# Performance work log

Measured on AMD Instinct MI355X. Metric: run time of the kernel, lower is better.

The kernel has to match this reference:

```python
import jax, jax.numpy as jnp
import numpy as np

B, N, D, HID, OUT = 4, 6144, 64, 512, 64
FINE_CONF = 0.25


def setup_inputs() -> dict:
    key = jax.random.key(0)
    ks = jax.random.split(key, 16)

    def unit(k, shape):
        v = jax.random.normal(k, shape, dtype=jnp.float32)
        return v / jnp.linalg.norm(v, axis=-1, keepdims=True)

    def lin(k, fan_in, shape):
        return jax.random.normal(k, shape, dtype=jnp.float32) * (1.0 / np.sqrt(fan_in))

    return {
        'feats1': unit(ks[0], (B, N, D)),
        'feats2': unit(ks[1], (B, N, D)),
        'kps1': jax.random.uniform(ks[2], (B, N, 2), dtype=jnp.float32) * 512.0,
        'kps2': jax.random.uniform(ks[3], (B, N, 2), dtype=jnp.float32) * 512.0,
        'scales1': jnp.ones((B, N), dtype=jnp.float32),
        'w1': lin(ks[4], 2 * D, (2 * D, HID)), 'b1': jnp.zeros((HID,), jnp.float32),
        'w2': lin(ks[5], HID, (HID, HID)),   'b2': jnp.zeros((HID,), jnp.float32),
        'w3': lin(ks[6], HID, (HID, HID)),   'b3': jnp.zeros((HID,), jnp.float32),
        'w4': lin(ks[7], HID, (HID, HID)),   'b4': jnp.zeros((HID,), jnp.float32),
        'w5': lin(ks[8], HID, (HID, OUT)),   'b5': jnp.zeros((OUT,), jnp.float32),
    }


def _fine_matcher(x, w1, b1, w2, b2, w3, b3, w4, b4, w5, b5):
    # eval-mode BN folded into the Linears -> plain MLP
    h = jax.nn.relu(x @ w1 + b1)
    h = jax.nn.relu(h @ w2 + b2)
    h = jax.nn.relu(h @ w3 + b3)
    h = jax.nn.relu(h @ w4 + b4)
    return h @ w5 + b5  # [B, N, 64]


def reference(feats1, feats2, kps1, kps2, scales1,
              w1, b1, w2, b2, w3, b3, w4, b4, w5, b5):
    # ---- batch_match: dense cosine sim + bidirectional argmax + mutual check ----
    cossim = jnp.einsum('bnd,bmd->bnm', feats1, feats2)       # [B, N, N]
    match12 = jnp.argmax(cossim, axis=-1)                      # [B, N]
    match21 = jnp.argmax(cossim, axis=1)                       # [B, N] (argmax over rows)
    idx0 = jnp.arange(match12.shape[1])
    back = jnp.take_along_axis(match21, match12, axis=1)       # match21[match12]
    mutual = back == idx0[None, :]                             # [B, N] bool

    # ---- refine_matches (masked instead of boolean compaction, jit-friendly) ----
    f2 = jnp.take_along_axis(feats2, match12[..., None], axis=1)   # [B, N, D]
    mkpts1 = jnp.take_along_axis(kps2, match12[..., None], axis=1) # [B, N, 2]
    offsets_raw = _fine_matcher(jnp.concatenate([feats1, f2], axis=-1),
                                w1, b1, w2, b2, w3, b3, w4, b4, w5, b5)  # [B, N, 64]

    # conf = softmax(3*offsets).max ; subpix uses softmax(3*offsets) too (temp=3)
    heat = jax.nn.softmax(3.0 * offsets_raw, axis=-1)          # [B, N, 64]
    conf = jnp.max(heat, axis=-1)                              # [B, N]

    hm = heat.reshape(heat.shape[0], heat.shape[1], 8, 8)      # [B, N, Hh, Wh]
    g = jnp.arange(8, dtype=heat.dtype) - 4.0                  # x - W//2 / y - H//2
    coords_x = jnp.sum(hm * g[None, None, None, :], axis=(-1, -2))
    coords_y = jnp.sum(hm * g[None, None, :, None], axis=(-1, -2))
    offsets = jnp.stack([coords_x, coords_y], axis=-1)         # [B, N, 2]

    mkpts0 = kps1 + offsets * scales1[..., None]
    matches = jnp.concatenate([mkpts0, mkpts1], axis=-1)       # [B, N, 4]
    mask_good = mutual & (conf > FINE_CONF)                    # valid-match mask
    return matches, mask_good
```

## Files before the change

### kernel.cpp

```cpp
#include <hip/hip_runtime.h>
#include <cstddef>
#include <cstdint>

#define BB 4
#define NN 6144
#define DD 64
#define HID 512
#define OUTD 64
#define CAP 512
#define RSPLIT 8

typedef unsigned long long ull;
typedef unsigned int u32;
typedef unsigned short u16;
typedef unsigned char u8;
typedef __attribute__((ext_vector_type(8))) short short8_t;
typedef __attribute__((ext_vector_type(4))) float floatx4;

#define OFF_ROWFIN 0
#define OFF_COLFIN 196608
#define OFF_WT     393216
#define OFF_F1T    2162688
#define OFF_F2T    5308416
#define OFF_RBM    8454144
#define OFF_CBM    10813440
#define OFF_CNTR   13172736
#define OFF_CNTC   13173504
#define OFF_LISTR  13174272
#define OFF_LISTC  13567488

#define WT1_OFF 0
#define WT2_OFF 65536
#define WT3_OFF 327680
#define WT4_OFF 589824
#define WT5_OFF 851968
#define WT_TOTAL 884736

__device__ __forceinline__ unsigned int fkey(float v) {
    unsigned int u = __float_as_uint(v);
    return (u & 0x80000000u) ? ~u : (u | 0x80000000u);
}

__device__ __forceinline__ float inv16(u32 k16) {
    u32 u = k16 << 16;
    return (u & 0x80000000u) ? __uint_as_float(u & 0x7fffffffu)
                             : __uint_as_float(~u);
}

__device__ __forceinline__ u16 f2bf(float f) {
    unsigned int u = __float_as_uint(f);
    u += 0x7FFFu + ((u >> 16) & 1u);
    return (u16)(u >> 16);
}

__device__ __forceinline__ u32 f2fp8x2(float a, float b) {
    return (u32)__builtin_amdgcn_cvt_pk_fp8_f32(a, b, 0, false) & 0xffffu;
}

__global__ __launch_bounds__(256) void prep_kernel(
    const float* __restrict__ w1, const float* __restrict__ w2,
    const float* __restrict__ w3, const float* __restrict__ w4,
    const float* __restrict__ w5,
    const float* __restrict__ f1, const float* __restrict__ f2,
    u8* __restrict__ wt8, u16* __restrict__ f1t, u16* __restrict__ f2t,
    ull* __restrict__ finals, int* __restrict__ cnts)
{
    int idx = blockIdx.x * 256 + threadIdx.x;

    if (idx < 2 * BB * NN) finals[idx] = 0ULL;
    if (idx < 384) cnts[idx] = 0;

    if (idx < WT_TOTAL) {
        const float* w; u8* o; int K, nsh, li;
        if (idx < 65536)        { w = w1; o = wt8 + WT1_OFF; K = 128; nsh = 9; li = idx; }
        else if (idx < 327680)  { w = w2; o = wt8 + WT2_OFF; K = 512; nsh = 9; li = idx - 65536; }
        else if (idx < 589824)  { w = w3; o = wt8 + WT3_OFF; K = 512; nsh = 9; li = idx - 327680; }
        else if (idx < 851968)  { w = w4; o = wt8 + WT4_OFF; K = 512; nsh = 9; li = idx - 589824; }
        else                    { w = w5; o = wt8 + WT5_OFF; K = 512; nsh = 6; li = idx - 851968; }
        int k = li >> nsh;
        int n = li & ((1 << nsh) - 1);
        u8 v = (u8)(f2fp8x2(w[li], 0.0f) & 0xff);
        int lane = (n & 15) | (((k >> 3) & 3) << 4);
        o[(((size_t)(n >> 4) * (K >> 5) + (k >> 5)) * 64 + lane) * 8 + (k & 7)] = v;
    }

    {
        const int TE = BB * NN * DD;
        const float* src; u16* dst; int e;
        if (idx < TE) { src = f1; dst = f1t; e = idx; }
        else          { src = f2; dst = f2t; e = idx - TE; }
        int k  = e & 63;
        int rn = e >> 6;
        int b  = rn / NN;
        int r  = rn - b * NN;
        int R  = r >> 7, rb = (r >> 4) & 7;
        int kb = k >> 5, lane = (r & 15) | (((k >> 3) & 3) << 4), j = k & 7;
        dst[(size_t)(b * 48 + R) * 8192 + ((rb * 2 + kb) * 64 + lane) * 8 + j] = f2bf(src[e]);
    }
}

__global__ __launch_bounds__(256, 2) void simb_kernel(
    const u16* __restrict__ f1t, const u16* __restrict__ f2t,
    u16* __restrict__ rbm, u16* __restrict__ cbm)
{
    __shared__ __align__(16) u16 sA[8192];
    __shared__ __align__(16) u16 sB[16384];
    __shared__ float cv[2][2][128];
    const int R = blockIdx.x, C2 = blockIdx.y, b = blockIdx.z;
    const int t = threadIdx.x, lane = t & 63, w = t >> 6;
    const int wr = w >> 1, wc = w & 1;
    const int l15 = lane & 15, l4 = lane >> 4;

    const u16* Ag = f1t + (size_t)(b * 48 + R) * 8192;
    const u16* Bg = f2t + (size_t)(b * 48 + C2 * 2) * 8192;

    #pragma unroll
    for (int rnd = 0; rnd < 4; ++rnd) {
        int c = rnd * 256 + t;
        *reinterpret_cast<uint4*>(&sA[c * 8]) = *reinterpret_cast<const uint4*>(Ag + c * 8);
    }
    #pragma unroll
    for (int rnd = 0; rnd < 8; ++rnd) {
        int c = rnd * 256 + t;
        *reinterpret_cast<uint4*>(&sB[c * 8]) = *reinterpret_cast<const uint4*>(Bg + c * 8);
    }
    __syncthreads();

    floatx4 acc[4][8];
    #pragma unroll
    for (int i = 0; i < 4; ++i)
        #pragma unroll
        for (int j = 0; j < 8; ++j) acc[i][j] = (floatx4)(0.0f);

    #pragma unroll
    for (int kb = 0; kb < 2; ++kb) {
        short8_t afr[4], bfr[8];
        #pragma unroll
        for (int i = 0; i < 4; ++i)
            afr[i] = *reinterpret_cast<const short8_t*>(
                &sA[(((wr * 4 + i) * 2 + kb) * 64 + lane) * 8]);
        #pragma unroll
        for (int j = 0; j < 8; ++j) {
            int cb = wc * 8 + j;
            bfr[j] = *reinterpret_cast<const short8_t*>(
                &sB[(cb >> 3) * 8192 + (((cb & 7) * 2 + kb) * 64 + lane) * 8]);
        }
        #pragma unroll
        for (int i = 0; i < 4; ++i)
            #pragma unroll
            for (int j = 0; j < 8; ++j)
                acc[i][j] = __builtin_amdgcn_mfma_f32_16x16x32_bf16(
                    afr[i], bfr[j], acc[i][j], 0, 0, 0);
    }

    const int Cme = C2 * 2 + wc;
    #pragma unroll
    for (int i = 0; i < 4; ++i) {
        #pragma unroll
        for (int reg = 0; reg < 4; ++reg) {
            float v = acc[i][0][reg];
            #pragma unroll
            for (int j = 1; j < 8; ++j) v = fmaxf(v, acc[i][j][reg]);
            v = fmaxf(v, __shfl_xor(v, 1));
            v = fmaxf(v, __shfl_xor(v, 2));
            v = fmaxf(v, __shfl_xor(v, 4));
            v = fmaxf(v, __shfl_xor(v, 8));
            if (l15 == 0) {
                int row = R * 128 + wr * 64 + i * 16 + l4 * 4 + reg;
                rbm[((size_t)b * NN + row) * 48 + Cme] = (u16)(fkey(v) >> 16);
            }
        }
    }

    #pragma unroll
    for (int j = 0; j < 8; ++j) {
        float v = acc[0][j][0];
        #pragma unroll
        for (int i = 0; i < 4; ++i)
            #pragma unroll
            for (int reg = 0; reg < 4; ++reg) v = fmaxf(v, acc[i][j][reg]);
        v = fmaxf(v, __shfl_xor(v, 16));
        v = fmaxf(v, __shfl_xor(v, 32));
        if (l4 == 0) cv[wc][wr][j * 16 + l15] = v;
    }
    __syncthreads();
    {
        int wcc = t >> 7, col0 = t & 127;
        float v = fmaxf(cv[wcc][0][col0], cv[wcc][1][col0]);
        int col = C2 * 256 + wcc * 128 + col0;
        cbm[((size_t)b * NN + col) * 48 + R] = (u16)(fkey(v) >> 16);
    }
}

__global__ __launch_bounds__(256) void scan_kernel(
    const u16* __restrict__ rbm, const u16* __restrict__ cbm,
    int* __restrict__ cntR, int* __restrict__ cntC,
    int* __restrict__ listR, int* __restrict__ listC)
{
    const u16* bm = blockIdx.y ? cbm : rbm;
    int* cnt  = blockIdx.y ? cntC : cntR;
    int* list = blockIdx.y ? listC : listR;

    __shared__ int lcnt[48];
    __shared__ int lbase[48];
    const int t = threadIdx.x;
    if (t < 48) lcnt[t] = 0;
    const int idx = blockIdx.x * 256 + t;
    const int b = (blockIdx.x * 256) / NN;
    const int n = idx - b * NN;

    u16 ks[48];
    const uint4* p4 = reinterpret_cast<const uint4*>(bm + (size_t)idx * 48);
    #pragma unroll
    for (int q = 0; q < 6; ++q) {
        uint4 u = p4[q];
        ks[q * 8 + 0] = (u16)(u.x & 0xffff); ks[q * 8 + 1] = (u16)(u.x >> 16);
        ks[q * 8 + 2] = (u16)(u.y & 0xffff); ks[q * 8 + 3] = (u16)(u.y >> 16);
        ks[q * 8 + 4] = (u16)(u.z & 0xffff); ks[q * 8 + 5] = (u16)(u.z >> 16);
        ks[q * 8 + 6] = (u16)(u.w & 0xffff); ks[q * 8 + 7] = (u16)(u.w >> 16);
    }
    u16 mx = 0;
    #pragma unroll
    for (int c = 0; c < 48; ++c) mx = ks[c] > mx ? ks[c] : mx;
    float thr = inv16(mx) - 0.010f;
    u32 m0 = 0, m1 = 0;
    #pragma unroll
    for (int c = 0; c < 48; ++c) {
        if (inv16((u32)ks[c] + 1) >= thr) {
            if (c < 32) m0 |= 1u << c; else m1 |= 1u << (c - 32);
        }
    }
    __syncthreads();
    {
        u32 a = m0;
        while (a) { int c = __builtin_ctz(a); a &= a - 1; atomicAdd(&lcnt[c], 1); }
        a = m1;
        while (a) { int c = 32 + __builtin_ctz(a); a &= a - 1; atomicAdd(&lcnt[c], 1); }
    }
    __syncthreads();
    if (t < 48) { lbase[t] = atomicAdd(&cnt[b * 48 + t], lcnt[t]); lcnt[t] = 0; }
    __syncthreads();
    {
        u32 a = m0;
        while (a) {
            int c = __builtin_ctz(a); a &= a - 1;
            int pos = lbase[c] + atomicAdd(&lcnt[c], 1);
            if (pos < CAP) list[(b * 48 + c) * CAP + pos] = n;
        }
        a = m1;
        while (a) {
            int c = 32 + __builtin_ctz(a); a &= a - 1;
            int pos = lbase[c] + atomicAdd(&lcnt[c], 1);
            if (pos < CAP) list[(b * 48 + c) * CAP + pos] = n;
        }
    }
}

__global__ __launch_bounds__(256, 2) void refine_kernel(
    const float* __restrict__ f1, const float* __restrict__ f2,
    const int* __restrict__ cntR, const int* __restrict__ cntC,
    const int* __restrict__ listR, const int* __restrict__ listC,
    ull* __restrict__ rowfin, ull* __restrict__ colfin)
{
    const float* qfeat = blockIdx.z ? f2 : f1;
    const float* tfeat = blockIdx.z ? f1 : f2;
    const int* cnt  = blockIdx.z ? cntC : cntR;
    const int* list = blockIdx.z ? listC : listR;
    ull* fin = blockIdx.z ? colfin : rowfin;

    const int b = blockIdx.x / 48;
    const int C = blockIdx.x - b * 48;
    const int sub = blockIdx.y;
    int n_items = cnt[b * 48 + C];
    if (n_items > CAP) n_items = CAP;
    int chunk = (n_items + RSPLIT - 1) / RSPLIT;
    int lo = sub * chunk;
    int hi = lo + chunk; if (hi > n_items) hi = n_items;
    if (lo >= hi) return;

    __shared__ float s2f[128 * 68];
    __shared__ float sq[16 * 68];
    const int t = threadIdx.x;
    const float* tb = tfeat + ((size_t)b * NN + C * 128) * 64;
    #pragma unroll
    for (int p = 0; p < 8; ++p) {
        int idx = p * 256 + t;
        int row = idx >> 4, c4 = idx & 15;
        *reinterpret_cast<float4*>(&s2f[row * 68 + c4 * 4]) =
            *reinterpret_cast<const float4*>(tb + row * 64 + c4 * 4);
    }
    __syncthreads();
    const int rs = t >> 4, cg = t & 15;
    const int* mylist = list + (b * 48 + C) * CAP;
    for (int base = lo; base < hi; base += 16) {
        {
            int lq = base + rs;
            int nn = (lq < hi) ? mylist[lq] : mylist[lo];
            *reinterpret_cast<float4*>(&sq[rs * 68 + cg * 4]) =
                *reinterpret_cast<const float4*>(qfeat + ((size_t)b * NN + nn) * 64 + cg * 4);
        }
        __syncthreads();

        int li = base + rs;
        bool valid = li < hi;
        int n = valid ? mylist[li] : mylist[lo];
        float dot[8];
        #pragma unroll
        for (int c8 = 0; c8 < 8; ++c8) dot[c8] = 0.0f;
        #pragma unroll 4
        for (int kq = 0; kq < 16; ++kq) {
            float4 a4 = *reinterpret_cast<const float4*>(&sq[rs * 68 + kq * 4]);
            #pragma unroll
            for (int c8 = 0; c8 < 8; ++c8) {
                float4 s4 = *reinterpret_cast<const float4*>(&s2f[(cg + 16 * c8) * 68 + kq * 4]);
                dot[c8] = fmaf(a4.x, s4.x, dot[c8]);
                dot[c8] = fmaf(a4.y, s4.y, dot[c8]);
                dot[c8] = fmaf(a4.z, s4.z, dot[c8]);
                dot[c8] = fmaf(a4.w, s4.w, dot[c8]);
            }
        }
        float bv = dot[0]; int bc = cg;
        #pragma unroll
        for (int c8 = 1; c8 < 8; ++c8) {
            if (dot[c8] > bv) { bv = dot[c8]; bc = cg + 16 * c8; }
        }
        ull pk = ((ull)fkey(bv) << 32) | (u32)(~(u32)(C * 128 + bc));
        ull qq;
        qq = __shfl_xor(pk, 1); pk = pk > qq ? pk : qq;
        qq = __shfl_xor(pk, 2); pk = pk > qq ? pk : qq;
        qq = __shfl_xor(pk, 4); pk = pk > qq ? pk : qq;
        qq = __shfl_xor(pk, 8); pk = pk > qq ? pk : qq;
        if (cg == 0 && valid) atomicMax(&fin[(size_t)b * NN + n], pk);
        __syncthreads();
    }
}


#define MLP_STEP(BUF, KB)                                                        \
    {                                                                            \
        const int kb2 = ((KB) + woff) & (NKB - 1);                               \
        __builtin_amdgcn_s_setprio(1);                                           \
        _Pragma("unroll")                                                        \
        for (int jb = 0; jb < 6; ++jb) {                                         \
            const int pt = jb * 16 + l15;                                        \
            const int sp = (kb2 * 4 + l4) ^ (pt & 7);                            \
            long bfr = *reinterpret_cast<const long*>(act + pt * 512 + sp * 8);  \
            _Pragma("unroll")                                                    \
            for (int ia = 0; ia < 4; ++ia)                                       \
                acc[ia][jb] = __builtin_amdgcn_mfma_f32_16x16x32_fp8_fp8(        \
                    BUF[ia], bfr, acc[ia][jb], 0, 0, 0);                         \
        }                                                                        \
        __builtin_amdgcn_s_setprio(0);                                           \
        if ((KB) + 3 < NKB) {                                                    \
            const int kbp = ((KB) + 3 + woff) & (NKB - 1);                       \
            _Pragma("unroll")                                                    \
            for (int ia = 0; ia < 4; ++ia)                                       \
                BUF[ia] = *reinterpret_cast<const long*>(                        \
                    wt8 + (((size_t)(chBlk0 + ia) * NKB + kbp) * 64 + lane) * 8);\
        }                                                                        \
    }

template<int K>
__device__ __forceinline__ void mlp_layer8(
    u8* act, const u8* __restrict__ wt8,
    const float* __restrict__ bias, int lane, int wid)
{
    constexpr int NKB = K / 32;
    floatx4 acc[4][6];
    #pragma unroll
    for (int ia = 0; ia < 4; ++ia)
        #pragma unroll
        for (int jb = 0; jb < 6; ++jb)
            acc[ia][jb] = (floatx4)(0.0f);

    const int l15 = lane & 15, l4 = lane >> 4;
    const int chBlk0 = wid * 4;
    const int woff = (wid * 2) & (NKB - 1);

    long a0[4], a1[4], a2[4];
    #pragma unroll
    for (int ia = 0; ia < 4; ++ia)
        a0[ia] = *reinterpret_cast<const long*>(
            wt8 + (((size_t)(chBlk0 + ia) * NKB + ((0 + woff) & (NKB - 1))) * 64 + lane) * 8);
    #pragma unroll
    for (int ia = 0; ia < 4; ++ia)
        a1[ia] = *reinterpret_cast<const long*>(
            wt8 + (((size_t)(chBlk0 + ia) * NKB + ((1 + woff) & (NKB - 1))) * 64 + lane) * 8);
    #pragma unroll
    for (int ia = 0; ia < 4; ++ia)
        a2[ia] = *reinterpret_cast<const long*>(
            wt8 + (((size_t)(chBlk0 + ia) * NKB + ((2 + woff) & (NKB - 1))) * 64 + lane) * 8);

    #pragma unroll
    for (int kb = 0; kb < NKB; ++kb) {
        if ((kb % 3) == 0)      MLP_STEP(a0, kb)
        else if ((kb % 3) == 1) MLP_STEP(a1, kb)
        else                    MLP_STEP(a2, kb)
    }
    __syncthreads();

    const int ch0 = wid * 64;
    #pragma unroll
    for (int ia = 0; ia < 4; ++ia) {
        int cb = ia * 16 + l4 * 4;
        float4 bv = *reinterpret_cast<const float4*>(bias + ch0 + cb);
        #pragma unroll
        for (int jb = 0; jb < 6; ++jb) {
            int pt = jb * 16 + l15;
            u32 pk0 = f2fp8x2(fmaxf(acc[ia][jb][0] + bv.x, 0.0f),
                              fmaxf(acc[ia][jb][1] + bv.y, 0.0f));
            u32 pk1 = f2fp8x2(fmaxf(acc[ia][jb][2] + bv.z, 0.0f),
                              fmaxf(acc[ia][jb][3] + bv.w, 0.0f));
            u32 word = pk0 | (pk1 << 16);
            int s = (ch0 + cb) >> 3;
            int sp = s ^ (pt & 7);
            *reinterpret_cast<u32*>(act + pt * 512 + sp * 8 + (cb & 4)) = word;
        }
    }
    __syncthreads();
}

__global__ __launch_bounds__(512, 2) void mlp_mfma_kernel(
    const float* __restrict__ f1, const float* __restrict__ f2,
    const float* __restrict__ kps1, const float* __restrict__ kps2,
    const float* __restrict__ scales1,
    const float* __restrict__ b1, const float* __restrict__ b2,
    const float* __restrict__ b3, const float* __restrict__ b4,
    const float* __restrict__ b5,
    const u8* __restrict__ wt8,
    const ull* __restrict__ rowfin, const ull* __restrict__ colfin,
    float* __restrict__ out)
{
    __shared__ __align__(16) unsigned char lds_raw[49152];
    u8* act = lds_raw;
    float* logf = reinterpret_cast<float*>(lds_raw);

    const int t = threadIdx.x;
    const int lane = t & 63, wid = t >> 6;
    const int base = blockIdx.x * 96;
    const int b = base / NN;
    const int n0 = base % NN;

    if (t < 384) {
        const int pt = t >> 2, seg = t & 3;
        const int n = n0 + pt;
        ull rm = rowfin[(size_t)b * NN + n];
        const int m = (int)(~(u32)(rm & 0xffffffffULL));
        const float* src = (seg < 2)
            ? (f1 + ((size_t)b * NN + n) * DD + seg * 32)
            : (f2 + ((size_t)b * NN + m) * DD + (seg - 2) * 32);
        #pragma unroll
        for (int q8 = 0; q8 < 4; ++q8) {
            float4 v0 = *reinterpret_cast<const float4*>(src + q8 * 8);
            float4 v1 = *reinterpret_cast<const float4*>(src + q8 * 8 + 4);
            ull w64 = (ull)f2fp8x2(v0.x, v0.y)
                    | ((ull)f2fp8x2(v0.z, v0.w) << 16)
                    | ((ull)f2fp8x2(v1.x, v1.y) << 32)
                    | ((ull)f2fp8x2(v1.z, v1.w) << 48);
            int s = seg * 4 + q8;
            int sp = s ^ (pt & 7);
            *reinterpret_cast<ull*>(act + pt * 512 + sp * 8) = w64;
        }
    }
    __syncthreads();

    mlp_layer8<128>(act, wt8 + WT1_OFF, b1, lane, wid);
    mlp_layer8<512>(act, wt8 + WT2_OFF, b2, lane, wid);
    mlp_layer8<512>(act, wt8 + WT3_OFF, b3, lane, wid);
    mlp_layer8<512>(act, wt8 + WT4_OFF, b4, lane, wid);

    {
        const int l15 = lane & 15, l4 = lane >> 4;
        floatx4 acc5[6];
        #pragma unroll
        for (int jb = 0; jb < 6; ++jb) acc5[jb] = (floatx4)(0.0f);
        if (wid < 4) {
            const int woff5 = (wid * 4) & 15;
            long a_cur = *reinterpret_cast<const long*>(
                wt8 + WT5_OFF + (((size_t)wid * 16 + woff5) * 64 + lane) * 8);
            long a_nxt;
            #pragma unroll
            for (int kb = 0; kb < 16; ++kb) {
                const int kb2 = (kb + woff5) & 15;
                if (kb + 1 < 16) {
                    const int kbn = (kb + 1 + woff5) & 15;
                    a_nxt = *reinterpret_cast<const long*>(
                        wt8 + WT5_OFF + (((size_t)wid * 16 + kbn) * 64 + lane) * 8);
                }
                __builtin_amdgcn_s_setprio(1);
                #pragma unroll
                for (int jb = 0; jb < 6; ++jb) {
                    const int pt = jb * 16 + l15;
                    const int sp = (kb2 * 4 + l4) ^ (pt & 7);
                    long bfr = *reinterpret_cast<const long*>(act + pt * 512 + sp * 8);
                    acc5[jb] = __builtin_amdgcn_mfma_f32_16x16x32_fp8_fp8(
                        a_cur, bfr, acc5[jb], 0, 0, 0);
                }
                __builtin_amdgcn_s_setprio(0);
                if (kb + 1 < 16) a_cur = a_nxt;
            }
        }
        __syncthreads();
        if (wid < 4) {
            int cb = wid * 16 + l4 * 4;
            float4 bv = *reinterpret_cast<const float4*>(b5 + cb);
            #pragma unroll
            for (int jb = 0; jb < 6; ++jb) {
                int pt = jb * 16 + l15;
                float4 o;
                o.x = acc5[jb][0] + bv.x;
                o.y = acc5[jb][1] + bv.y;
                o.z = acc5[jb][2] + bv.z;
                o.w = acc5[jb][3] + bv.w;
                *reinterpret_cast<float4*>(&logf[pt * 68 + cb]) = o;
            }
        }
        __syncthreads();
    }

    if (t < 96) {
        const int pt = t;
        const int n = n0 + pt;
        const float* lrow = &logf[pt * 68];
        float mx = -1e30f;
        #pragma unroll 8
        for (int j = 0; j < OUTD; ++j) mx = fmaxf(mx, 3.0f * lrow[j]);
        float s = 0.0f, cx = 0.0f, cy = 0.0f;
        #pragma unroll 8
        for (int j = 0; j < OUTD; ++j) {
            float e = __expf(3.0f * lrow[j] - mx);
            s  += e;
            cx += e * (float)((j & 7) - 4);
            cy += e * (float)((j >> 3) - 4);
        }
        float conf = 1.0f / s;
        cx /= s; cy /= s;
        ull rm = rowfin[(size_t)b * NN + n];
        int m = (int)(~(u32)(rm & 0xffffffffULL));
        ull cm = colfin[(size_t)b * NN + m];
        int back = (int)(~(u32)(cm & 0xffffffffULL));
        bool mutual = (back == n);
        float sc = scales1[(size_t)b * NN + n];
        float x0 = kps1[((size_t)b * NN + n) * 2 + 0] + cx * sc;
        float y0 = kps1[((size_t)b * NN + n) * 2 + 1] + cy * sc;
        float x1 = kps2[((size_t)b * NN + m) * 2 + 0];
        float y1 = kps2[((size_t)b * NN + m) * 2 + 1];
        float* mt = out + ((size_t)b * NN + n) * 4;
        mt[0] = x0; mt[1] = y0; mt[2] = x1; mt[3] = y1;
        out[(size_t)BB * NN * 4 + (size_t)b * NN + n] =
            (mutual && conf > 0.25f) ? 1.0f : 0.0f;
    }
}

extern "C" void kernel_launch(void* const* d_in, const int* in_sizes, int n_in,
                              void* d_out, int out_size, void* d_ws, size_t ws_size,
                              hipStream_t stream)
{
    const float* f1  = (const float*)d_in[0];
    const float* f2  = (const float*)d_in[1];
    const float* kp1 = (const float*)d_in[2];
    const float* kp2 = (const float*)d_in[3];
    const float* sc1 = (const float*)d_in[4];
    const float* w1  = (const float*)d_in[5];
    const float* b1  = (const float*)d_in[6];
    const float* w2  = (const float*)d_in[7];
    const float* b2  = (const float*)d_in[8];
    const float* w3  = (const float*)d_in[9];
    const float* b3  = (const float*)d_in[10];
    const float* w4  = (const float*)d_in[11];
    const float* b4  = (const float*)d_in[12];
    const float* w5  = (const float*)d_in[13];
    const float* b5  = (const float*)d_in[14];

    char* ws = (char*)d_ws;
    ull* rowfin = (ull*)(ws + OFF_ROWFIN);
    ull* colfin = (ull*)(ws + OFF_COLFIN);
    u8*  wt8    = (u8*)(ws + OFF_WT);
    u16* f1t    = (u16*)(ws + OFF_F1T);
    u16* f2t    = (u16*)(ws + OFF_F2T);
    u16* rbm    = (u16*)(ws + OFF_RBM);
    u16* cbm    = (u16*)(ws + OFF_CBM);
    int* cntR   = (int*)(ws + OFF_CNTR);
    int* cntC   = (int*)(ws + OFF_CNTC);
    int* listR  = (int*)(ws + OFF_LISTR);
    int* listC  = (int*)(ws + OFF_LISTC);
    float* out  = (float*)d_out;

    prep_kernel<<<(2 * BB * NN * DD) / 256, 256, 0, stream>>>(
        w1, w2, w3, w4, w5, f1, f2, wt8, f1t, f2t, rowfin, cntR);

    dim3 gS(48, 24, BB);
    simb_kernel<<<gS, 256, 0, stream>>>(f1t, f2t, rbm, cbm);

    dim3 gScan((BB * NN) / 256, 2);
    scan_kernel<<<gScan, 256, 0, stream>>>(rbm, cbm, cntR, cntC, listR, listC);

    dim3 gR(BB * 48, RSPLIT, 2);
    refine_kernel<<<gR, 256, 0, stream>>>(f1, f2, cntR, cntC, listR, listC,
                                          rowfin, colfin);

    mlp_mfma_kernel<<<(BB * NN) / 96, 512, 0, stream>>>(
        f1, f2, kp1, kp2, sc1, b1, b2, b3, b4, b5, wt8, rowfin, colfin, out);
}
```

Baseline: 157.1 us.

## Shrink similarity tile to 128x128 and transpose block-max layout for coalesced scan

The similarity-block kernel now computes a 128x128 tile per block instead of 128x256. Each wave owns 32 rows across all 128 columns, which halves LDS use and accumulators and doubles the grid, with launch bounds raised to target four blocks per CU. The row and column block-max arrays move from [row][48] to [48][row] layout, so both the simb stores and the scan kernel's per-column loads are coalesced across threads. The cost is twice the B-tile traffic for each A tile and 48 scalar u16 loads per thread in the scan instead of six vector loads.

```diff
diff --git a/kernel.cpp b/kernel.cpp
--- a/kernel.cpp
+++ b/kernel.cpp
@@ -99,63 +99,54 @@
     }
 }
 
-__global__ __launch_bounds__(256, 2) void simb_kernel(
+__global__ __launch_bounds__(256, 4) void simb_kernel(
     const u16* __restrict__ f1t, const u16* __restrict__ f2t,
     u16* __restrict__ rbm, u16* __restrict__ cbm)
 {
     __shared__ __align__(16) u16 sA[8192];
-    __shared__ __align__(16) u16 sB[16384];
-    __shared__ float cv[2][2][128];
-    const int R = blockIdx.x, C2 = blockIdx.y, b = blockIdx.z;
+    __shared__ __align__(16) u16 sB[8192];
+    __shared__ float cv[4][128];
+    const int R = blockIdx.x, C = blockIdx.y, b = blockIdx.z;
     const int t = threadIdx.x, lane = t & 63, w = t >> 6;
-    const int wr = w >> 1, wc = w & 1;
     const int l15 = lane & 15, l4 = lane >> 4;
 
     const u16* Ag = f1t + (size_t)(b * 48 + R) * 8192;
-    const u16* Bg = f2t + (size_t)(b * 48 + C2 * 2) * 8192;
+    const u16* Bg = f2t + (size_t)(b * 48 + C) * 8192;
 
     #pragma unroll
     for (int rnd = 0; rnd < 4; ++rnd) {
         int c = rnd * 256 + t;
         *reinterpret_cast<uint4*>(&sA[c * 8]) = *reinterpret_cast<const uint4*>(Ag + c * 8);
-    }
-    #pragma unroll
-    for (int rnd = 0; rnd < 8; ++rnd) {
-        int c = rnd * 256 + t;
         *reinterpret_cast<uint4*>(&sB[c * 8]) = *reinterpret_cast<const uint4*>(Bg + c * 8);
     }
     __syncthreads();
 
-    floatx4 acc[4][8];
-    #pragma unroll
-    for (int i = 0; i < 4; ++i)
+    floatx4 acc[2][8];
+    #pragma unroll
+    for (int i = 0; i < 2; ++i)
         #pragma unroll
         for (int j = 0; j < 8; ++j) acc[i][j] = (floatx4)(0.0f);
 
     #pragma unroll
     for (int kb = 0; kb < 2; ++kb) {
-        short8_t afr[4], bfr[8];
-        #pragma unroll
-        for (int i = 0; i < 4; ++i)
+        short8_t afr[2];
+        #pragma unroll
+        for (int i = 0; i < 2; ++i)
             afr[i] = *reinterpret_cast<const short8_t*>(
-                &sA[(((wr * 4 + i) * 2 + kb) * 64 + lane) * 8]);
+                &sA[(((2 * w + i) * 2 + kb) * 64 + lane) * 8]);
         #pragma unroll
         for (int j = 0; j < 8; ++j) {
-            int cb = wc * 8 + j;
-            bfr[j] = *reinterpret_cast<const short8_t*>(
-                &sB[(cb >> 3) * 8192 + (((cb & 7) * 2 + kb) * 64 + lane) * 8]);
-        }
-        #pragma unroll
-        for (int i = 0; i < 4; ++i)
+            short8_t bfr = *reinterpret_cast<const short8_t*>(
+                &sB[((j * 2 + kb) * 64 + lane) * 8]);
             #pragma unroll
-            for (int j = 0; j < 8; ++j)
+            for (int i = 0; i < 2; ++i)
                 acc[i][j] = __builtin_amdgcn_mfma_f32_16x16x32_bf16(
-                    afr[i], bfr[j], acc[i][j], 0, 0, 0);
-    }
-
-    const int Cme = C2 * 2 + wc;
-    #pragma unroll
-    for (int i = 0; i < 4; ++i) {
+                    afr[i], bfr, acc[i][j], 0, 0, 0);
+        }
+    }
+
+    #pragma unroll
+    for (int i = 0; i < 2; ++i) {
         #pragma unroll
         for (int reg = 0; reg < 4; ++reg) {
             float v = acc[i][0][reg];
@@ -166,8 +157,8 @@
             v = fmaxf(v, __shfl_xor(v, 4));
             v = fmaxf(v, __shfl_xor(v, 8));
             if (l15 == 0) {
-                int row = R * 128 + wr * 64 + i * 16 + l4 * 4 + reg;
-                rbm[((size_t)b * NN + row) * 48 + Cme] = (u16)(fkey(v) >> 16);
+                int row = R * 128 + w * 32 + i * 16 + l4 * 4 + reg;
+                rbm[((size_t)b * 48 + C) * NN + row] = (u16)(fkey(v) >> 16);
             }
         }
     }
@@ -176,19 +167,17 @@
     for (int j = 0; j < 8; ++j) {
         float v = acc[0][j][0];
         #pragma unroll
-        for (int i = 0; i < 4; ++i)
+        for (int i = 0; i < 2; ++i)
             #pragma unroll
             for (int reg = 0; reg < 4; ++reg) v = fmaxf(v, acc[i][j][reg]);
         v = fmaxf(v, __shfl_xor(v, 16));
         v = fmaxf(v, __shfl_xor(v, 32));
-        if (l4 == 0) cv[wc][wr][j * 16 + l15] = v;
-    }
-    __syncthreads();
-    {
-        int wcc = t >> 7, col0 = t & 127;
-        float v = fmaxf(cv[wcc][0][col0], cv[wcc][1][col0]);
-        int col = C2 * 256 + wcc * 128 + col0;
-        cbm[((size_t)b * NN + col) * 48 + R] = (u16)(fkey(v) >> 16);
+        if (l4 == 0) cv[w][j * 16 + l15] = v;
+    }
+    __syncthreads();
+    if (t < 128) {
+        float v = fmaxf(fmaxf(cv[0][t], cv[1][t]), fmaxf(cv[2][t], cv[3][t]));
+        cbm[((size_t)b * 48 + R) * NN + C * 128 + t] = (u16)(fkey(v) >> 16);
     }
 }
 
@@ -210,15 +199,10 @@
     const int n = idx - b * NN;
 
     u16 ks[48];
-    const uint4* p4 = reinterpret_cast<const uint4*>(bm + (size_t)idx * 48);
-    #pragma unroll
-    for (int q = 0; q < 6; ++q) {
-        uint4 u = p4[q];
-        ks[q * 8 + 0] = (u16)(u.x & 0xffff); ks[q * 8 + 1] = (u16)(u.x >> 16);
-        ks[q * 8 + 2] = (u16)(u.y & 0xffff); ks[q * 8 + 3] = (u16)(u.y >> 16);
-        ks[q * 8 + 4] = (u16)(u.z & 0xffff); ks[q * 8 + 5] = (u16)(u.z >> 16);
-        ks[q * 8 + 6] = (u16)(u.w & 0xffff); ks[q * 8 + 7] = (u16)(u.w >> 16);
-    }
+    #pragma unroll
+    for (int c = 0; c < 48; ++c)
+        ks[c] = bm[((size_t)b * 48 + c) * NN + n];
+
     u16 mx = 0;
     #pragma unroll
     for (int c = 0; c < 48; ++c) mx = ks[c] > mx ? ks[c] : mx;
@@ -589,7 +573,7 @@
     prep_kernel<<<(2 * BB * NN * DD) / 256, 256, 0, stream>>>(
         w1, w2, w3, w4, w5, f1, f2, wt8, f1t, f2t, rowfin, cntR);
 
-    dim3 gS(48, 24, BB);
+    dim3 gS(48, 48, BB);
     simb_kernel<<<gS, 256, 0, stream>>>(f1t, f2t, rbm, cbm);
 
     dim3 gScan((BB * NN) / 256, 2);
```

New measurement: 139.9 us. -11.0%, faster.
